# Kernel tuning notes

Measured on AMD Instinct MI355X. Metric: run time of the kernel, lower is better.

The kernel has to match this reference:

```python
import jax, jax.numpy as jnp
import numpy as np

D_MODEL = 1024
N_HEADS = 16
D_HEAD = D_MODEL // N_HEADS


def setup_inputs() -> dict:
    key = jax.random.key(0)
    k_x, k_wqkv, k_bqkv, k_wout, k_bout = jax.random.split(key, 5)
    x = jax.random.normal(k_x, (4, 2048, D_MODEL), dtype=jnp.float32)
    s = 1.0 / np.sqrt(D_MODEL)
    W_qkv = jax.random.uniform(k_wqkv, (D_MODEL, 3 * D_MODEL), jnp.float32, -s, s)
    b_qkv = jax.random.uniform(k_bqkv, (3 * D_MODEL,), jnp.float32, -s, s)
    W_out = jax.random.uniform(k_wout, (D_MODEL, D_MODEL), jnp.float32, -s, s)
    b_out = jax.random.uniform(k_bout, (D_MODEL,), jnp.float32, -s, s)
    return {"x": x, "W_qkv": W_qkv, "b_qkv": b_qkv, "W_out": W_out, "b_out": b_out}


def reference(x, W_qkv, b_qkv, W_out, b_out):
    B, S, _ = x.shape
    qkv = x @ W_qkv + b_qkv                      # [B,S,3*d_model]
    qkv = qkv.reshape(B, S, N_HEADS, 3 * D_HEAD).transpose(0, 2, 1, 3)  # [B,H,S,3*dh]
    q, k, v = jnp.split(qkv, 3, axis=-1)          # each [B,H,S,dh]
    scale = 1.0 / jnp.sqrt(jnp.asarray(D_HEAD, x.dtype))
    scores = jnp.einsum("bhqd,bhkd->bhqk", q, k) * scale  # [B,H,S,S]
    attn_weights = jax.nn.softmax(scores, axis=-1)
    attn = jnp.einsum("bhqk,bhkd->bhqd", attn_weights, v)  # [B,H,S,dh]
    attn = attn.transpose(0, 2, 1, 3).reshape(B, S, D_MODEL)
    return attn @ W_out + b_out
```

## Files before the change

kernel.cpp:

```cpp
#include <hip/hip_runtime.h>

typedef unsigned short u16;
typedef __bf16 bf16x8 __attribute__((ext_vector_type(8)));
typedef __bf16 bf16x4 __attribute__((ext_vector_type(4)));
typedef short s16x4 __attribute__((ext_vector_type(4)));
typedef float f32x4 __attribute__((ext_vector_type(4)));

union U4B8 { uint4 u; bf16x8 v; u16 s[8]; };
union U2S4 { uint2 u2; s16x4 s; bf16x4 h; };

__device__ __forceinline__ u16 f2b(float f) {
  union { float f; unsigned u; } x; x.f = f;
  unsigned u = x.u + 0x7fffu + ((x.u >> 16) & 1u);
  return (u16)(u >> 16);
}

__global__ __launch_bounds__(256) void cvt_f32_bf16(const float* __restrict__ in,
                                                    u16* __restrict__ out) {
  int i = blockIdx.x * 256 + threadIdx.x;
  float4 v = ((const float4*)in)[i];
  ushort4 h;
  h.x = f2b(v.x); h.y = f2b(v.y); h.z = f2b(v.z); h.w = f2b(v.w);
  ((ushort4*)out)[i] = h;
}

__global__ __launch_bounds__(256) void transpose_w(const float* __restrict__ in,
                                                   u16* __restrict__ out, int K, int N) {
  __shared__ u16 t[64 * 72];
  int k0 = blockIdx.y * 64, n0 = blockIdx.x * 64;
  int tid = threadIdx.x;
#pragma unroll
  for (int p = 0; p < 4; ++p) {
    int idx = p * 256 + tid;
    int k = idx >> 4, ng = idx & 15;
    float4 v = *(const float4*)(in + (k0 + k) * N + n0 + ng * 4);
    t[(ng * 4 + 0) * 72 + k] = f2b(v.x);
    t[(ng * 4 + 1) * 72 + k] = f2b(v.y);
    t[(ng * 4 + 2) * 72 + k] = f2b(v.z);
    t[(ng * 4 + 3) * 72 + k] = f2b(v.w);
  }
  __syncthreads();
#pragma unroll
  for (int p = 0; p < 2; ++p) {
    int idx = p * 256 + tid;
    int n = idx >> 3, kg = (idx & 7) * 8;
    uint4 u = *(uint4*)(&t[n * 72 + kg]);
    *(uint4*)(out + (n0 + n) * K + k0 + kg) = u;
  }
}

template <int MODE>
__global__ __launch_bounds__(256) void gemm_bf16(const u16* __restrict__ A,
                                                 const u16* __restrict__ B,
                                                 const float* __restrict__ bias,
                                                 float* __restrict__ outf,
                                                 u16* __restrict__ Qo, u16* __restrict__ Ko,
                                                 u16* __restrict__ Vo) {
  __shared__ u16 a_lds[128 * 32];
  __shared__ u16 b_lds[128 * 32];
  int tid = threadIdx.x;
  int l = tid & 63, w = tid >> 6;
  int wr = (w >> 1) * 64, wc = (w & 1) * 64;
  int m0 = blockIdx.y * 128, n0 = blockIdx.x * 128;
  int r15 = l & 15;
  int ka = (l >> 4) * 8;
  int r0 = tid >> 2, kg0 = (tid & 3) * 8;
  f32x4 acc[4][4] = {};
  for (int kt = 0; kt < 32; ++kt) {
    int k0 = kt * 32;
    __syncthreads();
    __builtin_amdgcn_global_load_lds(
        (const __attribute__((address_space(1))) void*)(A + (m0 + r0) * 1024 + k0 + kg0),
        (__attribute__((address_space(3))) void*)(&a_lds[tid * 8]), 16, 0, 0);
    __builtin_amdgcn_global_load_lds(
        (const __attribute__((address_space(1))) void*)(A + (m0 + 64 + r0) * 1024 + k0 + kg0),
        (__attribute__((address_space(3))) void*)(&a_lds[2048 + tid * 8]), 16, 0, 0);
    __builtin_amdgcn_global_load_lds(
        (const __attribute__((address_space(1))) void*)(B + (n0 + r0) * 1024 + k0 + kg0),
        (__attribute__((address_space(3))) void*)(&b_lds[tid * 8]), 16, 0, 0);
    __builtin_amdgcn_global_load_lds(
        (const __attribute__((address_space(1))) void*)(B + (n0 + 64 + r0) * 1024 + k0 + kg0),
        (__attribute__((address_space(3))) void*)(&b_lds[2048 + tid * 8]), 16, 0, 0);
    __syncthreads();
    bf16x8 af[4], bf[4];
#pragma unroll
    for (int i = 0; i < 4; ++i) {
      U4B8 ua; ua.u = *(uint4*)(&a_lds[(wr + i * 16 + r15) * 32 + ka]); af[i] = ua.v;
      U4B8 ub; ub.u = *(uint4*)(&b_lds[(wc + i * 16 + r15) * 32 + ka]); bf[i] = ub.v;
    }
#pragma unroll
    for (int i = 0; i < 4; ++i)
#pragma unroll
      for (int j = 0; j < 4; ++j)
        acc[i][j] = __builtin_amdgcn_mfma_f32_16x16x32_bf16(af[i], bf[j], acc[i][j], 0, 0, 0);
  }
  int rbase = (l >> 4) * 4;
#pragma unroll
  for (int i = 0; i < 4; ++i)
#pragma unroll
    for (int j = 0; j < 4; ++j) {
      int n = n0 + wc + j * 16 + r15;
      float bv = bias[n];
#pragma unroll
      for (int r = 0; r < 4; ++r) {
        int m = m0 + wr + i * 16 + rbase + r;
        float val = acc[i][j][r] + bv;
        if (MODE == 0) {
          int h = n / 192, rem = n % 192;
          int part = rem >> 6, d = rem & 63;
          int b = m >> 11, s = m & 2047;
          int off = (((b * 16 + h) * 2048) + s) * 64 + d;
          u16 hv = f2b(part == 0 ? val * 0.180336880111f : val);
          if (part == 0) Qo[off] = hv;
          else if (part == 1) Ko[off] = hv;
          else Vo[off] = hv;
        } else {
          outf[m * 1024 + n] = val;
        }
      }
    }
}

__global__ __launch_bounds__(512, 2) void attn_fwd(const u16* __restrict__ Q,
                                                   const u16* __restrict__ K,
                                                   const u16* __restrict__ V,
                                                   u16* __restrict__ O) {
  __shared__ u16 lds[16384];
  int tid = threadIdx.x;
  int l = tid & 63, w = tid >> 6;
  int g = l >> 4, r15 = l & 15, r7 = r15 & 7;
  int bid = blockIdx.x;
  int qb = (bid >> 3) & 7;
  int bh = (bid & 7) * 8 + (bid >> 6);
  const u16* Kb = K + bh * 131072;
  const u16* Vb = V + bh * 131072;
  int ka = g * 8;
  int qbase = qb * 256 + w * 32;
  U4B8 t0, t1, t2, t3;
  t0.u = *(const uint4*)(Q + bh * 131072 + (qbase + r15) * 64 + ka);
  t1.u = *(const uint4*)(Q + bh * 131072 + (qbase + r15) * 64 + 32 + ka);
  t2.u = *(const uint4*)(Q + bh * 131072 + (qbase + 16 + r15) * 64 + ka);
  t3.u = *(const uint4*)(Q + bh * 131072 + (qbase + 16 + r15) * 64 + 32 + ka);
  bf16x8 qf00 = t0.v, qf01 = t1.v, qf10 = t2.v, qf11 = t3.v;

  int kaddr[4];
#pragma unroll
  for (int c = 0; c < 4; ++c) kaddr[c] = (c * 16 + r15) * 64 + ((g ^ r7) << 3);
  int vaddr0[4];
#pragma unroll
  for (int dq = 0; dq < 4; ++dq) {
    int d = r15 + 16 * dq;
    int vsw = ((d >> 3) ^ d) & 15;
    vaddr0[dq] = 8192 + d * 64 + ((g ^ vsw) << 2);
  }

  int krow0 = tid >> 3;
  int kcg = (((tid & 7) ^ (krow0 & 7)) << 3);
  int sr0 = tid >> 3, sdg = (tid & 7) * 8;
  int vwa[8];
#pragma unroll
  for (int i = 0; i < 8; ++i) {
    int d = sdg + i;
    int sw = ((d >> 3) ^ d) & 15;
    vwa[i] = 8192 + d * 64 + ((((sr0 >> 2)) ^ sw) << 2) + (sr0 & 3);
  }
  U4B8 vreg;

#define STAGE(OFFW, TN)                                                                    \
  {                                                                                        \
    int kv0 = (TN) * 64;                                                                   \
    __builtin_amdgcn_global_load_lds(                                                      \
        (const __attribute__((address_space(1))) void*)(Kb + (kv0 + krow0) * 64 + kcg),    \
        (__attribute__((address_space(3))) void*)(&lds[(OFFW) + tid * 8]), 16, 0, 0);      \
    vreg.u = *(const uint4*)(Vb + (kv0 + sr0) * 64 + sdg);                                 \
  }

#define WRITEV(OFFW)                                                                       \
  {                                                                                        \
    _Pragma("unroll") for (int i = 0; i < 8; ++i) {                                        \
      lds[(OFFW) + vwa[i]] = vreg.s[i];                                                    \
    }                                                                                      \
  }

  float l0 = 0.f, l1 = 0.f;
  f32x4 o0[4] = {}, o1[4] = {};

#define COMPUTE(OFFR)                                                                      \
  {                                                                                        \
    _Pragma("unroll") for (int c = 0; c < 4; ++c) {                                        \
      U4B8 k0, k1;                                                                         \
      k0.u = *(const uint4*)(&lds[(OFFR) + kaddr[c]]);                                     \
      k1.u = *(const uint4*)(&lds[(OFFR) + (kaddr[c] ^ 32)]);                              \
      f32x4 z0 = {}, z1 = {};                                                              \
      z0 = __builtin_amdgcn_mfma_f32_16x16x32_bf16(k0.v, qf00, z0, 0, 0, 0);               \
      z0 = __builtin_amdgcn_mfma_f32_16x16x32_bf16(k1.v, qf01, z0, 0, 0, 0);               \
      z1 = __builtin_amdgcn_mfma_f32_16x16x32_bf16(k0.v, qf10, z1, 0, 0, 0);               \
      z1 = __builtin_amdgcn_mfma_f32_16x16x32_bf16(k1.v, qf11, z1, 0, 0, 0);               \
      float a0 = __builtin_amdgcn_exp2f(z0[0]), a1 = __builtin_amdgcn_exp2f(z0[1]);        \
      float a2 = __builtin_amdgcn_exp2f(z0[2]), a3 = __builtin_amdgcn_exp2f(z0[3]);        \
      l0 += (a0 + a1) + (a2 + a3);                                                         \
      U2S4 pa0;                                                                            \
      pa0.h[0] = (__bf16)a0; pa0.h[1] = (__bf16)a1;                                        \
      pa0.h[2] = (__bf16)a2; pa0.h[3] = (__bf16)a3;                                        \
      float b0 = __builtin_amdgcn_exp2f(z1[0]), b1 = __builtin_amdgcn_exp2f(z1[1]);        \
      float b2 = __builtin_amdgcn_exp2f(z1[2]), b3 = __builtin_amdgcn_exp2f(z1[3]);        \
      l1 += (b0 + b1) + (b2 + b3);                                                         \
      U2S4 pa1;                                                                            \
      pa1.h[0] = (__bf16)b0; pa1.h[1] = (__bf16)b1;                                        \
      pa1.h[2] = (__bf16)b2; pa1.h[3] = (__bf16)b3;                                        \
      _Pragma("unroll") for (int dq = 0; dq < 4; ++dq) {                                   \
        U2S4 vb;                                                                           \
        vb.u2 = *(const uint2*)(&lds[(OFFR) + (vaddr0[dq] ^ (16 * c))]);                   \
        o0[dq] = __builtin_amdgcn_mfma_f32_16x16x16bf16_1k(pa0.s, vb.s, o0[dq], 0, 0, 0);  \
        o1[dq] = __builtin_amdgcn_mfma_f32_16x16x16bf16_1k(pa1.s, vb.s, o1[dq], 0, 0, 0);  \
      }                                                                                    \
    }                                                                                      \
  }

  STAGE(0, 0);
  WRITEV(0);
#pragma unroll 1
  for (int tt = 0; tt < 16; ++tt) {
    __syncthreads();
    STAGE(4096, 2 * tt + 1);
    COMPUTE(0);
    WRITEV(4096);
    __syncthreads();
    if (tt < 15) STAGE(0, 2 * tt + 2);
    COMPUTE(4096);
    if (tt < 15) WRITEV(0);
  }
#undef STAGE
#undef WRITEV
#undef COMPUTE

  l0 += __shfl_xor(l0, 16); l0 += __shfl_xor(l0, 32);
  l1 += __shfl_xor(l1, 16); l1 += __shfl_xor(l1, 32);
  float i0 = 1.f / l0, i1 = 1.f / l1;
  float c0[4], c1[4];
#pragma unroll
  for (int j = 0; j < 4; ++j) {
    c0[j] = __shfl(i0, 4 * g + j);
    c1[j] = __shfl(i1, 4 * g + j);
  }
  __syncthreads();
  u16* stg = lds + w * 2048;
#pragma unroll
  for (int j = 0; j < 4; ++j) {
    int rr0 = 4 * g + j;
    int rr1 = 16 + 4 * g + j;
#pragma unroll
    for (int dq = 0; dq < 4; ++dq) {
      int pc = ((dq ^ g) << 4) + r15;
      stg[rr0 * 64 + pc] = f2b(o0[dq][j] * c0[j]);
      stg[rr1 * 64 + pc] = f2b(o1[dq][j] * c1[j]);
    }
  }
  int b = bh >> 4, h = bh & 15;
  int colpair = (l & 31) * 2;
  int rowsel = l >> 5;
#pragma unroll
  for (int it = 0; it < 16; ++it) {
    int rr = 2 * it + rowsel;
    int phys = rr * 64 + (((colpair >> 4) ^ ((rr >> 2) & 3)) << 4) + (colpair & 15);
    unsigned pv = *(const unsigned*)(&stg[phys]);
    int row = qbase + rr;
    *(unsigned*)(&O[(b * 2048 + row) * 1024 + h * 64 + colpair]) = pv;
  }
}

extern "C" void kernel_launch(void* const* d_in, const int* in_sizes, int n_in,
                              void* d_out, int out_size, void* d_ws, size_t ws_size,
                              hipStream_t stream) {
  const float* x = (const float*)d_in[0];
  const float* Wqkv = (const float*)d_in[1];
  const float* bqkv = (const float*)d_in[2];
  const float* Wout = (const float*)d_in[3];
  const float* bout = (const float*)d_in[4];
  float* out = (float*)d_out;

  u16* ws = (u16*)d_ws;
  u16* WtQ = ws;
  u16* WtO = WtQ + 3072 * 1024;
  u16* Xb  = WtO + 1024 * 1024;
  u16* Qw  = Xb + 8192 * 1024;
  u16* Kw  = Qw + 64 * 2048 * 64;
  u16* Vw  = Kw + 64 * 2048 * 64;
  u16* Aw  = Vw + 64 * 2048 * 64;

  cvt_f32_bf16<<<8192, 256, 0, stream>>>(x, Xb);
  transpose_w<<<dim3(48, 16), 256, 0, stream>>>(Wqkv, WtQ, 1024, 3072);
  transpose_w<<<dim3(16, 16), 256, 0, stream>>>(Wout, WtO, 1024, 1024);
  gemm_bf16<0><<<dim3(24, 64), 256, 0, stream>>>(Xb, WtQ, bqkv, nullptr, Qw, Kw, Vw);
  attn_fwd<<<512, 512, 0, stream>>>(Qw, Kw, Vw, Aw);
  gemm_bf16<1><<<dim3(8, 64), 256, 0, stream>>>(Aw, WtO, bout, out, nullptr, nullptr, nullptr);
}
```

Before: 212.5 us.

## Merge prep kernels, triple-buffer GEMM loads, widen attention per-wave query tile

Three prep kernels (x conversion and two weight transposes) become one launch that dispatches on block index, saving two launch gaps. The GEMM moves to a three-buffer LDS pipeline: it issues the next tile's loads before computing the current one and waits with vmcnt instead of a full barrier pair. The attention kernel halves threads per block to 256, so each wave now handles 64 query rows (four fragments) and reuses each K/V LDS read across more MFMAs. The cost is higher register pressure in attention and more LDS per GEMM block, which may reduce occupancy.

```diff
diff --git a/kernel.cpp b/kernel.cpp
--- a/kernel.cpp
+++ b/kernel.cpp
@@ -15,20 +15,30 @@
   return (u16)(u >> 16);
 }
 
-__global__ __launch_bounds__(256) void cvt_f32_bf16(const float* __restrict__ in,
-                                                    u16* __restrict__ out) {
-  int i = blockIdx.x * 256 + threadIdx.x;
-  float4 v = ((const float4*)in)[i];
-  ushort4 h;
-  h.x = f2b(v.x); h.y = f2b(v.y); h.z = f2b(v.z); h.w = f2b(v.w);
-  ((ushort4*)out)[i] = h;
-}
-
-__global__ __launch_bounds__(256) void transpose_w(const float* __restrict__ in,
-                                                   u16* __restrict__ out, int K, int N) {
+__global__ __launch_bounds__(256) void prep(const float* __restrict__ x,
+                                            const float* __restrict__ Wqkv,
+                                            const float* __restrict__ Wout,
+                                            u16* __restrict__ Xb,
+                                            u16* __restrict__ WtQ,
+                                            u16* __restrict__ WtO) {
   __shared__ u16 t[64 * 72];
-  int k0 = blockIdx.y * 64, n0 = blockIdx.x * 64;
+  int bid = blockIdx.x;
   int tid = threadIdx.x;
+  if (bid < 8192) {
+    int i = bid * 256 + tid;
+    float4 v = ((const float4*)x)[i];
+    ushort4 h;
+    h.x = f2b(v.x); h.y = f2b(v.y); h.z = f2b(v.z); h.w = f2b(v.w);
+    ((ushort4*)Xb)[i] = h;
+    return;
+  }
+  const float* in; u16* out; int N, bx, by;
+  if (bid < 8960) {
+    int tt = bid - 8192; bx = tt % 48; by = tt / 48; in = Wqkv; out = WtQ; N = 3072;
+  } else {
+    int tt = bid - 8960; bx = tt & 15; by = tt >> 4; in = Wout; out = WtO; N = 1024;
+  }
+  int k0 = by * 64, n0 = bx * 64;
 #pragma unroll
   for (int p = 0; p < 4; ++p) {
     int idx = p * 256 + tid;
@@ -45,7 +55,7 @@
     int idx = p * 256 + tid;
     int n = idx >> 3, kg = (idx & 7) * 8;
     uint4 u = *(uint4*)(&t[n * 72 + kg]);
-    *(uint4*)(out + (n0 + n) * K + k0 + kg) = u;
+    *(uint4*)(out + (n0 + n) * 1024 + k0 + kg) = u;
   }
 }
 
@@ -56,8 +66,8 @@
                                                  float* __restrict__ outf,
                                                  u16* __restrict__ Qo, u16* __restrict__ Ko,
                                                  u16* __restrict__ Vo) {
-  __shared__ u16 a_lds[128 * 32];
-  __shared__ u16 b_lds[128 * 32];
+  __shared__ u16 a_lds[3 * 4096];
+  __shared__ u16 b_lds[3 * 4096];
   int tid = threadIdx.x;
   int l = tid & 63, w = tid >> 6;
   int wr = (w >> 1) * 64, wc = (w & 1) * 64;
@@ -66,34 +76,53 @@
   int ka = (l >> 4) * 8;
   int r0 = tid >> 2, kg0 = (tid & 3) * 8;
   f32x4 acc[4][4] = {};
+
+#define STAGE_G(BUF, KT)                                                                     \
+  {                                                                                          \
+    int kk = (KT) * 32;                                                                      \
+    __builtin_amdgcn_global_load_lds(                                                        \
+        (const __attribute__((address_space(1))) void*)(A + (m0 + r0) * 1024 + kk + kg0),    \
+        (__attribute__((address_space(3))) void*)(&a_lds[(BUF) * 4096 + tid * 8]), 16, 0, 0);\
+    __builtin_amdgcn_global_load_lds(                                                        \
+        (const __attribute__((address_space(1))) void*)(A + (m0 + 64 + r0) * 1024 + kk + kg0),\
+        (__attribute__((address_space(3))) void*)(&a_lds[(BUF) * 4096 + 2048 + tid * 8]), 16, 0, 0);\
+    __builtin_amdgcn_global_load_lds(                                                        \
+        (const __attribute__((address_space(1))) void*)(B + (n0 + r0) * 1024 + kk + kg0),    \
+        (__attribute__((address_space(3))) void*)(&b_lds[(BUF) * 4096 + tid * 8]), 16, 0, 0);\
+    __builtin_amdgcn_global_load_lds(                                                        \
+        (const __attribute__((address_space(1))) void*)(B + (n0 + 64 + r0) * 1024 + kk + kg0),\
+        (__attribute__((address_space(3))) void*)(&b_lds[(BUF) * 4096 + 2048 + tid * 8]), 16, 0, 0);\
+  }
+
+  STAGE_G(0, 0);
+  int cur = 0;
+#pragma unroll 1
   for (int kt = 0; kt < 32; ++kt) {
-    int k0 = kt * 32;
-    __syncthreads();
-    __builtin_amdgcn_global_load_lds(
-        (const __attribute__((address_space(1))) void*)(A + (m0 + r0) * 1024 + k0 + kg0),
-        (__attribute__((address_space(3))) void*)(&a_lds[tid * 8]), 16, 0, 0);
-    __builtin_amdgcn_global_load_lds(
-        (const __attribute__((address_space(1))) void*)(A + (m0 + 64 + r0) * 1024 + k0 + kg0),
-        (__attribute__((address_space(3))) void*)(&a_lds[2048 + tid * 8]), 16, 0, 0);
-    __builtin_amdgcn_global_load_lds(
-        (const __attribute__((address_space(1))) void*)(B + (n0 + r0) * 1024 + k0 + kg0),
-        (__attribute__((address_space(3))) void*)(&b_lds[tid * 8]), 16, 0, 0);
-    __builtin_amdgcn_global_load_lds(
-        (const __attribute__((address_space(1))) void*)(B + (n0 + 64 + r0) * 1024 + k0 + kg0),
-        (__attribute__((address_space(3))) void*)(&b_lds[2048 + tid * 8]), 16, 0, 0);
-    __syncthreads();
+    int nxt = (cur == 2) ? 0 : cur + 1;
+    if (kt < 31) {
+      STAGE_G(nxt, kt + 1);
+      asm volatile("s_waitcnt vmcnt(4)" ::: "memory");
+    } else {
+      asm volatile("s_waitcnt vmcnt(0)" ::: "memory");
+    }
+    __builtin_amdgcn_s_barrier();
+    __builtin_amdgcn_sched_barrier(0);
+    int bo = cur * 4096;
     bf16x8 af[4], bf[4];
 #pragma unroll
     for (int i = 0; i < 4; ++i) {
-      U4B8 ua; ua.u = *(uint4*)(&a_lds[(wr + i * 16 + r15) * 32 + ka]); af[i] = ua.v;
-      U4B8 ub; ub.u = *(uint4*)(&b_lds[(wc + i * 16 + r15) * 32 + ka]); bf[i] = ub.v;
+      U4B8 ua; ua.u = *(uint4*)(&a_lds[bo + (wr + i * 16 + r15) * 32 + ka]); af[i] = ua.v;
+      U4B8 ub; ub.u = *(uint4*)(&b_lds[bo + (wc + i * 16 + r15) * 32 + ka]); bf[i] = ub.v;
     }
 #pragma unroll
     for (int i = 0; i < 4; ++i)
 #pragma unroll
       for (int j = 0; j < 4; ++j)
         acc[i][j] = __builtin_amdgcn_mfma_f32_16x16x32_bf16(af[i], bf[j], acc[i][j], 0, 0, 0);
-  }
+    cur = nxt;
+  }
+#undef STAGE_G
+
   int rbase = (l >> 4) * 4;
 #pragma unroll
   for (int i = 0; i < 4; ++i)
@@ -121,7 +150,7 @@
     }
 }
 
-__global__ __launch_bounds__(512, 2) void attn_fwd(const u16* __restrict__ Q,
+__global__ __launch_bounds__(256, 2) void attn_fwd(const u16* __restrict__ Q,
                                                    const u16* __restrict__ K,
                                                    const u16* __restrict__ V,
                                                    u16* __restrict__ O) {
@@ -135,13 +164,15 @@
   const u16* Kb = K + bh * 131072;
   const u16* Vb = V + bh * 131072;
   int ka = g * 8;
-  int qbase = qb * 256 + w * 32;
-  U4B8 t0, t1, t2, t3;
-  t0.u = *(const uint4*)(Q + bh * 131072 + (qbase + r15) * 64 + ka);
-  t1.u = *(const uint4*)(Q + bh * 131072 + (qbase + r15) * 64 + 32 + ka);
-  t2.u = *(const uint4*)(Q + bh * 131072 + (qbase + 16 + r15) * 64 + ka);
-  t3.u = *(const uint4*)(Q + bh * 131072 + (qbase + 16 + r15) * 64 + 32 + ka);
-  bf16x8 qf00 = t0.v, qf01 = t1.v, qf10 = t2.v, qf11 = t3.v;
+  int qbase = qb * 256 + w * 64;
+  bf16x8 qfr[4][2];
+#pragma unroll
+  for (int f = 0; f < 4; ++f) {
+    U4B8 ta, tb;
+    ta.u = *(const uint4*)(Q + bh * 131072 + (qbase + 16 * f + r15) * 64 + ka);
+    tb.u = *(const uint4*)(Q + bh * 131072 + (qbase + 16 * f + r15) * 64 + 32 + ka);
+    qfr[f][0] = ta.v; qfr[f][1] = tb.v;
+  }
 
   int kaddr[4];
 #pragma unroll
@@ -164,7 +195,7 @@
     int sw = ((d >> 3) ^ d) & 15;
     vwa[i] = 8192 + d * 64 + ((((sr0 >> 2)) ^ sw) << 2) + (sr0 & 3);
   }
-  U4B8 vreg;
+  U4B8 vreg0, vreg1;
 
 #define STAGE(OFFW, TN)                                                                    \
   {                                                                                        \
@@ -172,18 +203,23 @@
     __builtin_amdgcn_global_load_lds(                                                      \
         (const __attribute__((address_space(1))) void*)(Kb + (kv0 + krow0) * 64 + kcg),    \
         (__attribute__((address_space(3))) void*)(&lds[(OFFW) + tid * 8]), 16, 0, 0);      \
-    vreg.u = *(const uint4*)(Vb + (kv0 + sr0) * 64 + sdg);                                 \
+    __builtin_amdgcn_global_load_lds(                                                      \
+        (const __attribute__((address_space(1))) void*)(Kb + (kv0 + krow0 + 32) * 64 + kcg), \
+        (__attribute__((address_space(3))) void*)(&lds[(OFFW) + 2048 + tid * 8]), 16, 0, 0); \
+    vreg0.u = *(const uint4*)(Vb + (kv0 + sr0) * 64 + sdg);                                \
+    vreg1.u = *(const uint4*)(Vb + (kv0 + sr0 + 32) * 64 + sdg);                           \
   }
 
 #define WRITEV(OFFW)                                                                       \
   {                                                                                        \
     _Pragma("unroll") for (int i = 0; i < 8; ++i) {                                        \
-      lds[(OFFW) + vwa[i]] = vreg.s[i];                                                    \
+      lds[(OFFW) + vwa[i]] = vreg0.s[i];                                                   \
+      lds[(OFFW) + (vwa[i] ^ 32)] = vreg1.s[i];                                            \
     }                                                                                      \
   }
 
-  float l0 = 0.f, l1 = 0.f;
-  f32x4 o0[4] = {}, o1[4] = {};
+  float lsum[4] = {0.f, 0.f, 0.f, 0.f};
+  f32x4 o[4][4] = {};
 
 #define COMPUTE(OFFR)                                                                      \
   {                                                                                        \
@@ -191,28 +227,24 @@
       U4B8 k0, k1;                                                                         \
       k0.u = *(const uint4*)(&lds[(OFFR) + kaddr[c]]);                                     \
       k1.u = *(const uint4*)(&lds[(OFFR) + (kaddr[c] ^ 32)]);                              \
-      f32x4 z0 = {}, z1 = {};                                                              \
-      z0 = __builtin_amdgcn_mfma_f32_16x16x32_bf16(k0.v, qf00, z0, 0, 0, 0);               \
-      z0 = __builtin_amdgcn_mfma_f32_16x16x32_bf16(k1.v, qf01, z0, 0, 0, 0);               \
-      z1 = __builtin_amdgcn_mfma_f32_16x16x32_bf16(k0.v, qf10, z1, 0, 0, 0);               \
-      z1 = __builtin_amdgcn_mfma_f32_16x16x32_bf16(k1.v, qf11, z1, 0, 0, 0);               \
-      float a0 = __builtin_amdgcn_exp2f(z0[0]), a1 = __builtin_amdgcn_exp2f(z0[1]);        \
-      float a2 = __builtin_amdgcn_exp2f(z0[2]), a3 = __builtin_amdgcn_exp2f(z0[3]);        \
-      l0 += (a0 + a1) + (a2 + a3);                                                         \
-      U2S4 pa0;                                                                            \
-      pa0.h[0] = (__bf16)a0; pa0.h[1] = (__bf16)a1;                                        \
-      pa0.h[2] = (__bf16)a2; pa0.h[3] = (__bf16)a3;                                        \
-      float b0 = __builtin_amdgcn_exp2f(z1[0]), b1 = __builtin_amdgcn_exp2f(z1[1]);        \
-      float b2 = __builtin_amdgcn_exp2f(z1[2]), b3 = __builtin_amdgcn_exp2f(z1[3]);        \
-      l1 += (b0 + b1) + (b2 + b3);                                                         \
-      U2S4 pa1;                                                                            \
-      pa1.h[0] = (__bf16)b0; pa1.h[1] = (__bf16)b1;                                        \
-      pa1.h[2] = (__bf16)b2; pa1.h[3] = (__bf16)b3;                                        \
+      U2S4 pa[4];                                                                          \
+      _Pragma("unroll") for (int f = 0; f < 4; ++f) {                                      \
+        f32x4 z = {};                                                                      \
+        z = __builtin_amdgcn_mfma_f32_16x16x32_bf16(k0.v, qfr[f][0], z, 0, 0, 0);          \
+        z = __builtin_amdgcn_mfma_f32_16x16x32_bf16(k1.v, qfr[f][1], z, 0, 0, 0);          \
+        float a0 = __builtin_amdgcn_exp2f(z[0]), a1 = __builtin_amdgcn_exp2f(z[1]);        \
+        float a2 = __builtin_amdgcn_exp2f(z[2]), a3 = __builtin_amdgcn_exp2f(z[3]);        \
+        lsum[f] += (a0 + a1) + (a2 + a3);                                                  \
+        pa[f].h[0] = (__bf16)a0; pa[f].h[1] = (__bf16)a1;                                  \
+        pa[f].h[2] = (__bf16)a2; pa[f].h[3] = (__bf16)a3;                                  \
+      }                                                                                    \
       _Pragma("unroll") for (int dq = 0; dq < 4; ++dq) {                                   \
         U2S4 vb;                                                                           \
         vb.u2 = *(const uint2*)(&lds[(OFFR) + (vaddr0[dq] ^ (16 * c))]);                   \
-        o0[dq] = __builtin_amdgcn_mfma_f32_16x16x16bf16_1k(pa0.s, vb.s, o0[dq], 0, 0, 0);  \
-        o1[dq] = __builtin_amdgcn_mfma_f32_16x16x16bf16_1k(pa1.s, vb.s, o1[dq], 0, 0, 0);  \
+        o[0][dq] = __builtin_amdgcn_mfma_f32_16x16x16bf16_1k(pa[0].s, vb.s, o[0][dq], 0, 0, 0);\
+        o[1][dq] = __builtin_amdgcn_mfma_f32_16x16x16bf16_1k(pa[1].s, vb.s, o[1][dq], 0, 0, 0);\
+        o[2][dq] = __builtin_amdgcn_mfma_f32_16x16x16bf16_1k(pa[2].s, vb.s, o[2][dq], 0, 0, 0);\
+        o[3][dq] = __builtin_amdgcn_mfma_f32_16x16x16bf16_1k(pa[3].s, vb.s, o[3][dq], 0, 0, 0);\
       }                                                                                    \
     }                                                                                      \
   }
@@ -234,33 +266,34 @@
 #undef WRITEV
 #undef COMPUTE
 
-  l0 += __shfl_xor(l0, 16); l0 += __shfl_xor(l0, 32);
-  l1 += __shfl_xor(l1, 16); l1 += __shfl_xor(l1, 32);
-  float i0 = 1.f / l0, i1 = 1.f / l1;
-  float c0[4], c1[4];
-#pragma unroll
-  for (int j = 0; j < 4; ++j) {
-    c0[j] = __shfl(i0, 4 * g + j);
-    c1[j] = __shfl(i1, 4 * g + j);
+  float cf[4][4];
+#pragma unroll
+  for (int f = 0; f < 4; ++f) {
+    float s = lsum[f];
+    s += __shfl_xor(s, 16);
+    s += __shfl_xor(s, 32);
+    float inv = 1.f / s;
+#pragma unroll
+    for (int j = 0; j < 4; ++j) cf[f][j] = __shfl(inv, 4 * g + j);
   }
   __syncthreads();
-  u16* stg = lds + w * 2048;
-#pragma unroll
-  for (int j = 0; j < 4; ++j) {
-    int rr0 = 4 * g + j;
-    int rr1 = 16 + 4 * g + j;
-#pragma unroll
-    for (int dq = 0; dq < 4; ++dq) {
-      int pc = ((dq ^ g) << 4) + r15;
-      stg[rr0 * 64 + pc] = f2b(o0[dq][j] * c0[j]);
-      stg[rr1 * 64 + pc] = f2b(o1[dq][j] * c1[j]);
+  u16* stg = lds + w * 4096;
+#pragma unroll
+  for (int f = 0; f < 4; ++f)
+#pragma unroll
+    for (int j = 0; j < 4; ++j) {
+      int rr = 16 * f + 4 * g + j;
+#pragma unroll
+      for (int dq = 0; dq < 4; ++dq) {
+        int pc = ((dq ^ g) << 4) + r15;
+        stg[rr * 64 + pc] = f2b(o[f][dq][j] * cf[f][j]);
+      }
     }
-  }
   int b = bh >> 4, h = bh & 15;
   int colpair = (l & 31) * 2;
   int rowsel = l >> 5;
 #pragma unroll
-  for (int it = 0; it < 16; ++it) {
+  for (int it = 0; it < 32; ++it) {
     int rr = 2 * it + rowsel;
     int phys = rr * 64 + (((colpair >> 4) ^ ((rr >> 2) & 3)) << 4) + (colpair & 15);
     unsigned pv = *(const unsigned*)(&stg[phys]);
@@ -288,10 +321,8 @@
   u16* Vw  = Kw + 64 * 2048 * 64;
   u16* Aw  = Vw + 64 * 2048 * 64;
 
-  cvt_f32_bf16<<<8192, 256, 0, stream>>>(x, Xb);
-  transpose_w<<<dim3(48, 16), 256, 0, stream>>>(Wqkv, WtQ, 1024, 3072);
-  transpose_w<<<dim3(16, 16), 256, 0, stream>>>(Wout, WtO, 1024, 1024);
+  prep<<<9216, 256, 0, stream>>>(x, Wqkv, Wout, Xb, WtQ, WtO);
   gemm_bf16<0><<<dim3(24, 64), 256, 0, stream>>>(Xb, WtQ, bqkv, nullptr, Qw, Kw, Vw);
-  attn_fwd<<<512, 512, 0, stream>>>(Qw, Kw, Vw, Aw);
+  attn_fwd<<<512, 256, 0, stream>>>(Qw, Kw, Vw, Aw);
   gemm_bf16<1><<<dim3(8, 64), 256, 0, stream>>>(Aw, WtO, bout, out, nullptr, nullptr, nullptr);
 }
```

After: 372.9 us. 1.75x slower.
